# Kernel tuning notes

Measured on AMD Instinct MI355X. Metric: run time of the kernel, lower is better.

Reference implementation:

```python
import jax, jax.numpy as jnp
import numpy as np

B, S, IN_DIM, D, OUT_DIM = 8, 2048, 256, 1024, 256

def setup_inputs() -> dict:
    key = jax.random.key(0)
    ks = jax.random.split(key, 11)
    s_in = 1.0 / np.sqrt(IN_DIM)
    s_d = 1.0 / np.sqrt(D)
    return {
        "x": jax.random.normal(ks[0], (B, S, IN_DIM), dtype=jnp.float32),
        "Wi": jax.random.uniform(ks[1], (IN_DIM, D), jnp.float32, -s_in, s_in),
        "bi": jax.random.uniform(ks[2], (D,), jnp.float32, -s_in, s_in),
        "Wq": jax.random.uniform(ks[3], (D, D), jnp.float32, -s_d, s_d),
        "bq": jax.random.uniform(ks[4], (D,), jnp.float32, -s_d, s_d),
        "Wk": jax.random.uniform(ks[5], (D, D), jnp.float32, -s_d, s_d),
        "bk": jax.random.uniform(ks[6], (D,), jnp.float32, -s_d, s_d),
        "Wv": jax.random.uniform(ks[7], (D, D), jnp.float32, -s_d, s_d),
        "bv": jax.random.uniform(ks[8], (D,), jnp.float32, -s_d, s_d),
        "Wo": jax.random.uniform(ks[9], (D, OUT_DIM), jnp.float32, -s_d, s_d),
        "bo": jax.random.uniform(ks[10], (OUT_DIM,), jnp.float32, -s_d, s_d),
    }

def reference(x, Wi, bi, Wq, bq, Wk, bk, Wv, bv, Wo, bo):
    h = jnp.einsum('bsi,id->bsd', x, Wi) + bi          # input projection
    Q = jnp.einsum('bsd,de->bse', h, Wq) + bq
    K = jnp.einsum('bsd,de->bse', h, Wk) + bk
    V = jnp.einsum('bsd,de->bse', h, Wv) + bv
    scale = 1.0 / jnp.sqrt(jnp.asarray(Q.shape[-1], h.dtype))
    scores = jnp.einsum('bqd,bkd->bqk', Q, K) * scale   # [B,S,S]
    weights = jax.nn.softmax(scores, axis=-1)
    attended = jnp.einsum('bqk,bkd->bqd', weights, V)
    last = attended[:, -1, :]                           # only last token is projected
    out = last @ Wo + bo                                # [B, OUT_DIM]
    return out
```

## Files before the change

kernel.cpp:

```cpp
#include <hip/hip_runtime.h>

typedef unsigned short u16;
typedef __attribute__((ext_vector_type(8))) short bf16x8;
typedef __attribute__((ext_vector_type(4))) float f32x4;

#define B_  8
#define S_  2048
#define IN_ 256
#define D_  1024
#define OUT_ 256
#define M_  (B_*S_)

#define OFF_WIT   0UL
#define OFF_H     524288UL
#define OFF_QPART 34078720UL
#define OFF_Q     34340864UL
#define OFF_U     34373632UL
#define OFF_SC    34406400UL
#define OFF_W     34471936UL
#define OFF_HPART 34537472UL
#define OFF_HBAR  35061760UL
#define OFF_APART 35094528UL
#define OFF_ABAR  35356672UL
#define OFF_OPART 35389440UL

static __device__ __forceinline__ float bf2f(u16 u) {
    union { unsigned i; float f; } x; x.i = ((unsigned)u) << 16; return x.f;
}
static __device__ __forceinline__ u16 f2bf(float f) {
    union { float f; unsigned i; } x; x.f = f;
    unsigned r = x.i + 0x7FFFu + ((x.i >> 16) & 1u);
    return (u16)(r >> 16);
}
static __device__ __forceinline__ float2 bf2x2(int p) {
    union { unsigned i; float f; } a, b;
    a.i = ((unsigned)p) << 16;
    b.i = ((unsigned)p) & 0xFFFF0000u;
    float2 r; r.x = a.f; r.y = b.f; return r;
}

__global__ __launch_bounds__(256) void k_wit(const float* __restrict__ Wi, u16* __restrict__ WiT) {
    __shared__ float t[64][65];
    const int tid = threadIdx.x;
    const int n0 = blockIdx.x * 64;
    const int k0 = blockIdx.y * 64;
    const int c = tid & 63, rr = tid >> 6;
#pragma unroll
    for (int p = 0; p < 16; ++p) {
        int r = p * 4 + rr;
        t[r][c] = Wi[(k0 + r) * 1024 + n0 + c];
    }
    __syncthreads();
#pragma unroll
    for (int p = 0; p < 16; ++p) {
        int n = p * 4 + rr;
        WiT[(n0 + n) * 256 + k0 + c] = f2bf(t[c][n]);
    }
}

__global__ __launch_bounds__(256) void k_hgemm(const float* __restrict__ x,
                                               const u16* __restrict__ WiT,
                                               const float* __restrict__ bi,
                                               u16* __restrict__ h) {
    __shared__ u16 lA[128 * 128];
    __shared__ u16 lB[128 * 128];
    const int tid = threadIdx.x;
    const int l = tid & 63, w = tid >> 6;
    const int wm = w >> 1, wn = w & 1;
    const int m0 = blockIdx.y * 128, n0 = blockIdx.x * 128;
    const int q = l >> 4, r = l & 15;

    f32x4 acc[4][4];
#pragma unroll
    for (int mt = 0; mt < 4; ++mt)
#pragma unroll
        for (int nt = 0; nt < 4; ++nt)
            acc[mt][nt] = (f32x4){0.f, 0.f, 0.f, 0.f};

    for (int kh = 0; kh < 2; ++kh) {
        if (kh) __syncthreads();
#pragma unroll
        for (int p = 0; p < 8; ++p) {
            int id = p * 256 + tid;
            int row = id >> 4, cb = id & 15;
            const float4* src = reinterpret_cast<const float4*>(&x[(m0 + row) * IN_ + kh * 128 + cb * 8]);
            float4 v0 = src[0], v1 = src[1];
            u16 tmp[8];
            tmp[0] = f2bf(v0.x); tmp[1] = f2bf(v0.y); tmp[2] = f2bf(v0.z); tmp[3] = f2bf(v0.w);
            tmp[4] = f2bf(v1.x); tmp[5] = f2bf(v1.y); tmp[6] = f2bf(v1.z); tmp[7] = f2bf(v1.w);
            int4 pk;
            pk.x = (int)tmp[0] | ((int)tmp[1] << 16);
            pk.y = (int)tmp[2] | ((int)tmp[3] << 16);
            pk.z = (int)tmp[4] | ((int)tmp[5] << 16);
            pk.w = (int)tmp[6] | ((int)tmp[7] << 16);
            *reinterpret_cast<int4*>(&lA[row * 128 + ((cb ^ (row & 7)) << 3)]) = pk;
        }
#pragma unroll
        for (int p = 0; p < 8; ++p) {
            int id = p * 256 + tid;
            int row = id >> 4, cb = id & 15;
            int4 v = *reinterpret_cast<const int4*>(&WiT[(n0 + row) * IN_ + kh * 128 + cb * 8]);
            *reinterpret_cast<int4*>(&lB[row * 128 + ((cb ^ (row & 7)) << 3)]) = v;
        }
        __syncthreads();
#pragma unroll
        for (int kk = 0; kk < 4; ++kk) {
            int cb = kk * 4 + q;
            bf16x8 af[4], bfr[4];
#pragma unroll
            for (int mt = 0; mt < 4; ++mt) {
                int row = wm * 64 + mt * 16 + r;
                af[mt] = *reinterpret_cast<const bf16x8*>(&lA[row * 128 + ((cb ^ (row & 7)) << 3)]);
            }
#pragma unroll
            for (int nt = 0; nt < 4; ++nt) {
                int row = wn * 64 + nt * 16 + r;
                bfr[nt] = *reinterpret_cast<const bf16x8*>(&lB[row * 128 + ((cb ^ (row & 7)) << 3)]);
            }
#pragma unroll
            for (int mt = 0; mt < 4; ++mt)
#pragma unroll
                for (int nt = 0; nt < 4; ++nt)
                    acc[mt][nt] = __builtin_amdgcn_mfma_f32_16x16x32_bf16(af[mt], bfr[nt], acc[mt][nt], 0, 0, 0);
        }
    }
#pragma unroll
    for (int nt = 0; nt < 4; ++nt) {
        int col = n0 + wn * 64 + nt * 16 + r;
        float bival = bi[col];
#pragma unroll
        for (int mt = 0; mt < 4; ++mt) {
#pragma unroll
            for (int j = 0; j < 4; ++j) {
                int row = m0 + wm * 64 + mt * 16 + q * 4 + j;
                h[(size_t)row * D_ + col] = f2bf(acc[mt][nt][j] + bival);
            }
        }
    }
}

__global__ __launch_bounds__(256) void k_qpart(const u16* __restrict__ h, const float* __restrict__ Wq,
                                               float* __restrict__ part) {
    const int ec = blockIdx.x, dc = blockIdx.y, b = blockIdx.z, tid = threadIdx.x;
    __shared__ float hl[128];
    if (tid < 128) hl[tid] = bf2f(h[((size_t)(b * S_ + S_ - 1)) * D_ + dc * 128 + tid]);
    __syncthreads();
    const int e = ec * 256 + tid;
    float acc = 0.f;
#pragma unroll 4
    for (int i = 0; i < 128; ++i)
        acc += hl[i] * Wq[(size_t)(dc * 128 + i) * D_ + e];
    part[(dc * 8 + b) * D_ + e] = acc;
}

__global__ __launch_bounds__(256) void k_qreduce(const float* __restrict__ part, const float* __restrict__ bq,
                                                 float* __restrict__ Q) {
    const int e = blockIdx.x * 256 + threadIdx.x, b = blockIdx.y;
    float s = bq[e];
#pragma unroll
    for (int dc = 0; dc < 8; ++dc) s += part[(dc * 8 + b) * D_ + e];
    Q[b * D_ + e] = s;
}

__global__ __launch_bounds__(256) void k_u(const float* __restrict__ Wk, const float* __restrict__ Q,
                                           float* __restrict__ u) {
    const int b = blockIdx.y;
    const int w = threadIdx.x >> 6, l = threadIdx.x & 63;
    const int dbase = blockIdx.x * 16 + w * 4;
    const float* qb = &Q[b * D_];
    float4 qv[4];
#pragma unroll
    for (int p = 0; p < 4; ++p) qv[p] = *reinterpret_cast<const float4*>(&qb[p * 256 + l * 4]);
#pragma unroll
    for (int i = 0; i < 4; ++i) {
        const int d = dbase + i;
        const float* wr = &Wk[(size_t)d * D_];
        float acc = 0.f;
#pragma unroll
        for (int p = 0; p < 4; ++p) {
            float4 wv = *reinterpret_cast<const float4*>(&wr[p * 256 + l * 4]);
            acc += wv.x * qv[p].x + wv.y * qv[p].y + wv.z * qv[p].z + wv.w * qv[p].w;
        }
#pragma unroll
        for (int s = 32; s > 0; s >>= 1) acc += __shfl_xor(acc, s);
        if (l == 0) u[b * D_ + d] = acc;
    }
}

__global__ __launch_bounds__(256) void k_scores(const u16* __restrict__ h, const float* __restrict__ u,
                                                float* __restrict__ sc) {
    const int b = blockIdx.y;
    const int k = blockIdx.x * 4 + (threadIdx.x >> 6);
    const int l = threadIdx.x & 63;
    const u16* hr = &h[(size_t)(b * S_ + k) * D_];
    const float* ur = &u[b * D_];
    float acc = 0.f;
#pragma unroll
    for (int p = 0; p < 4; ++p) {
        int off = p * 256 + l * 4;
        int2 hv = *reinterpret_cast<const int2*>(&hr[off]);
        float4 uv = *reinterpret_cast<const float4*>(&ur[off]);
        float2 p0 = bf2x2(hv.x), p1 = bf2x2(hv.y);
        acc += p0.x * uv.x + p0.y * uv.y + p1.x * uv.z + p1.y * uv.w;
    }
#pragma unroll
    for (int s = 32; s > 0; s >>= 1) acc += __shfl_xor(acc, s);
    if (l == 0) sc[b * S_ + k] = acc * 0.03125f;
}

__global__ __launch_bounds__(256) void k_softmax(const float* __restrict__ sc, float* __restrict__ wt) {
    const int b = blockIdx.x, tid = threadIdx.x;
    const int w = tid >> 6, l = tid & 63;
    __shared__ float red[4], red2[4];
    float s[8];
    float mx = -1e30f;
#pragma unroll
    for (int j = 0; j < 8; ++j) {
        s[j] = sc[b * S_ + j * 256 + tid];
        mx = fmaxf(mx, s[j]);
    }
#pragma unroll
    for (int t = 32; t > 0; t >>= 1) mx = fmaxf(mx, __shfl_xor(mx, t));
    if (l == 0) red[w] = mx;
    __syncthreads();
    float bm = fmaxf(fmaxf(red[0], red[1]), fmaxf(red[2], red[3]));
    float sum = 0.f;
#pragma unroll
    for (int j = 0; j < 8; ++j) {
        s[j] = expf(s[j] - bm);
        sum += s[j];
    }
#pragma unroll
    for (int t = 32; t > 0; t >>= 1) sum += __shfl_xor(sum, t);
    if (l == 0) red2[w] = sum;
    __syncthreads();
    float inv = 1.f / (red2[0] + red2[1] + red2[2] + red2[3]);
#pragma unroll
    for (int j = 0; j < 8; ++j) wt[b * S_ + j * 256 + tid] = s[j] * inv;
}

__global__ __launch_bounds__(256) void k_hpart(const u16* __restrict__ h, const float* __restrict__ wt,
                                               float* __restrict__ part) {
    const int kc = blockIdx.x, b = blockIdx.y, tid = threadIdx.x;
    const int d0 = tid * 4;
    float a0 = 0.f, a1 = 0.f, a2 = 0.f, a3 = 0.f;
    for (int k = kc * 128; k < kc * 128 + 128; ++k) {
        float wgt = wt[b * S_ + k];
        int2 hv = *reinterpret_cast<const int2*>(&h[(size_t)(b * S_ + k) * D_ + d0]);
        float2 p0 = bf2x2(hv.x), p1 = bf2x2(hv.y);
        a0 += wgt * p0.x; a1 += wgt * p0.y; a2 += wgt * p1.x; a3 += wgt * p1.y;
    }
    float4 st = {a0, a1, a2, a3};
    *reinterpret_cast<float4*>(&part[(kc * 8 + b) * D_ + d0]) = st;
}

__global__ __launch_bounds__(256) void k_hreduce(const float* __restrict__ part, float* __restrict__ hbar) {
    const int d = blockIdx.x * 256 + threadIdx.x, b = blockIdx.y;
    float s = 0.f;
#pragma unroll
    for (int kc = 0; kc < 16; ++kc) s += part[(kc * 8 + b) * D_ + d];
    hbar[b * D_ + d] = s;
}

__global__ __launch_bounds__(256) void k_apart(const float* __restrict__ hbar, const float* __restrict__ Wv,
                                               float* __restrict__ part) {
    const int ec = blockIdx.x, dc = blockIdx.y, b = blockIdx.z, tid = threadIdx.x;
    __shared__ float hl[128];
    if (tid < 128) hl[tid] = hbar[b * D_ + dc * 128 + tid];
    __syncthreads();
    const int e = ec * 256 + tid;
    float acc = 0.f;
#pragma unroll 4
    for (int i = 0; i < 128; ++i)
        acc += hl[i] * Wv[(size_t)(dc * 128 + i) * D_ + e];
    part[(dc * 8 + b) * D_ + e] = acc;
}

__global__ __launch_bounds__(256) void k_areduce(const float* __restrict__ part, const float* __restrict__ bv,
                                                 float* __restrict__ abar) {
    const int e = blockIdx.x * 256 + threadIdx.x, b = blockIdx.y;
    float s = bv[e];
#pragma unroll
    for (int dc = 0; dc < 8; ++dc) s += part[(dc * 8 + b) * D_ + e];
    abar[b * D_ + e] = s;
}

__global__ __launch_bounds__(256) void k_opart(const float* __restrict__ abar, const float* __restrict__ Wo,
                                               float* __restrict__ part) {
    const int dc = blockIdx.x, b = blockIdx.y, tid = threadIdx.x;
    __shared__ float al[256];
    al[tid] = abar[b * D_ + dc * 256 + tid];
    __syncthreads();
    float acc = 0.f;
#pragma unroll 4
    for (int i = 0; i < 256; ++i)
        acc += al[i] * Wo[(size_t)(dc * 256 + i) * OUT_ + tid];
    part[(dc * 8 + b) * OUT_ + tid] = acc;
}

__global__ __launch_bounds__(256) void k_oreduce(const float* __restrict__ part, const float* __restrict__ bo,
                                                 float* __restrict__ out) {
    const int b = blockIdx.x, tid = threadIdx.x;
    float s = bo[tid];
#pragma unroll
    for (int dc = 0; dc < 4; ++dc) s += part[(dc * 8 + b) * OUT_ + tid];
    out[b * OUT_ + tid] = s;
}

extern "C" void kernel_launch(void* const* d_in, const int* in_sizes, int n_in,
                              void* d_out, int out_size, void* d_ws, size_t ws_size,
                              hipStream_t stream) {
    const float* x  = (const float*)d_in[0];
    const float* Wi = (const float*)d_in[1];
    const float* bi = (const float*)d_in[2];
    const float* Wq = (const float*)d_in[3];
    const float* bq = (const float*)d_in[4];
    const float* Wk = (const float*)d_in[5];
    const float* Wv = (const float*)d_in[7];
    const float* bv = (const float*)d_in[8];
    const float* Wo = (const float*)d_in[9];
    const float* bo = (const float*)d_in[10];
    float* out = (float*)d_out;

    char* ws = (char*)d_ws;
    u16*   WiT   = (u16*)  (ws + OFF_WIT);
    u16*   h     = (u16*)  (ws + OFF_H);
    float* Qpart = (float*)(ws + OFF_QPART);
    float* Q     = (float*)(ws + OFF_Q);
    float* u     = (float*)(ws + OFF_U);
    float* sc    = (float*)(ws + OFF_SC);
    float* wt    = (float*)(ws + OFF_W);
    float* hpart = (float*)(ws + OFF_HPART);
    float* hbar  = (float*)(ws + OFF_HBAR);
    float* apart = (float*)(ws + OFF_APART);
    float* abar  = (float*)(ws + OFF_ABAR);
    float* opart = (float*)(ws + OFF_OPART);

    k_wit    <<<dim3(16, 4),    256, 0, stream>>>(Wi, WiT);
    k_hgemm  <<<dim3(8, 128),   256, 0, stream>>>(x, WiT, bi, h);
    k_qpart  <<<dim3(4, 8, 8),  256, 0, stream>>>(h, Wq, Qpart);
    k_qreduce<<<dim3(4, 8),     256, 0, stream>>>(Qpart, bq, Q);
    k_u      <<<dim3(64, 8),    256, 0, stream>>>(Wk, Q, u);
    k_scores <<<dim3(512, 8),   256, 0, stream>>>(h, u, sc);
    k_softmax<<<dim3(8),        256, 0, stream>>>(sc, wt);
    k_hpart  <<<dim3(16, 8),    256, 0, stream>>>(h, wt, hpart);
    k_hreduce<<<dim3(4, 8),     256, 0, stream>>>(hpart, hbar);
    k_apart  <<<dim3(4, 8, 8),  256, 0, stream>>>(hbar, Wv, apart);
    k_areduce<<<dim3(4, 8),     256, 0, stream>>>(apart, bv, abar);
    k_opart  <<<dim3(4, 8),     256, 0, stream>>>(abar, Wo, opart);
    k_oreduce<<<dim3(8),        256, 0, stream>>>(opart, bo, out);
}
```

Before: 184.6 us.

## Fold Wq·Wk and Wv·Wo products, fuse softmax and collapse to five kernels

Reassociates attention for the last query: precomputes Wq·Wk^T and Wv·Wo with MFMA GEMMs inside the h-projection launch, and folds biases into constant vectors (dropping bk, which cancels in softmax). Scores, a chunked online softmax and weighted h accumulation are fused into one kernel, with a final kernel merging chunk maxima/sums and applying the folded output matrix. This removes many small GEMV and reduction launches and the repeated fp32 weight streaming, at the cost of extra dense GEMM work and bf16 rounding of weight products.

```diff
diff --git a/kernel.cpp b/kernel.cpp
--- a/kernel.cpp
+++ b/kernel.cpp
@@ -4,25 +4,25 @@
 typedef __attribute__((ext_vector_type(8))) short bf16x8;
 typedef __attribute__((ext_vector_type(4))) float f32x4;
 
-#define B_  8
-#define S_  2048
-#define IN_ 256
-#define D_  1024
+#define B_   8
+#define S_   2048
+#define IN_  256
+#define D_   1024
 #define OUT_ 256
-#define M_  (B_*S_)
+#define KC_  32
+#define RC_  64
 
 #define OFF_WIT   0UL
-#define OFF_H     524288UL
-#define OFF_QPART 34078720UL
-#define OFF_Q     34340864UL
-#define OFF_U     34373632UL
-#define OFF_SC    34406400UL
-#define OFF_W     34471936UL
-#define OFF_HPART 34537472UL
-#define OFF_HBAR  35061760UL
-#define OFF_APART 35094528UL
-#define OFF_ABAR  35356672UL
-#define OFF_OPART 35389440UL
+#define OFF_WOT   524288UL
+#define OFF_H     1048576UL
+#define OFF_AMAT  34603008UL
+#define OFF_AWO   38797312UL
+#define OFF_C     39845888UL
+#define OFF_CVOP  39849984UL
+#define OFF_CVO   39866368UL
+#define OFF_U     39870464UL
+#define OFF_PART  39903232UL
+#define OFF_MSUM  40951808UL
 
 static __device__ __forceinline__ float bf2f(u16 u) {
     union { unsigned i; float f; } x; x.i = ((unsigned)u) << 16; return x.f;
@@ -39,68 +39,113 @@
     float2 r; r.x = a.f; r.y = b.f; return r;
 }
 
-__global__ __launch_bounds__(256) void k_wit(const float* __restrict__ Wi, u16* __restrict__ WiT) {
+__global__ __launch_bounds__(256) void k1(const float* __restrict__ Wi, u16* __restrict__ WiT,
+                                          const float* __restrict__ Wo, u16* __restrict__ WoT,
+                                          const float* __restrict__ Wk, const float* __restrict__ bq,
+                                          float* __restrict__ cvec,
+                                          const float* __restrict__ bv, float* __restrict__ cvop) {
     __shared__ float t[64][65];
-    const int tid = threadIdx.x;
-    const int n0 = blockIdx.x * 64;
-    const int k0 = blockIdx.y * 64;
-    const int c = tid & 63, rr = tid >> 6;
-#pragma unroll
-    for (int p = 0; p < 16; ++p) {
-        int r = p * 4 + rr;
-        t[r][c] = Wi[(k0 + r) * 1024 + n0 + c];
-    }
-    __syncthreads();
-#pragma unroll
-    for (int p = 0; p < 16; ++p) {
-        int n = p * 4 + rr;
-        WiT[(n0 + n) * 256 + k0 + c] = f2bf(t[c][n]);
-    }
-}
-
-__global__ __launch_bounds__(256) void k_hgemm(const float* __restrict__ x,
-                                               const u16* __restrict__ WiT,
-                                               const float* __restrict__ bi,
-                                               u16* __restrict__ h) {
-    __shared__ u16 lA[128 * 128];
-    __shared__ u16 lB[128 * 128];
+    const int blk = blockIdx.x, tid = threadIdx.x;
+    if (blk < 64) {
+        const int n0 = (blk & 15) * 64, k0 = (blk >> 4) * 64;
+        const int cc = tid & 63, rr = tid >> 6;
+#pragma unroll
+        for (int p = 0; p < 16; ++p) { int r = p * 4 + rr; t[r][cc] = Wi[(k0 + r) * 1024 + n0 + cc]; }
+        __syncthreads();
+#pragma unroll
+        for (int p = 0; p < 16; ++p) { int n = p * 4 + rr; WiT[(n0 + n) * 256 + k0 + cc] = f2bf(t[cc][n]); }
+    } else if (blk < 128) {
+        const int b2 = blk - 64;
+        const int e0 = (b2 & 15) * 64, o0 = (b2 >> 4) * 64;
+        const int cc = tid & 63, rr = tid >> 6;
+#pragma unroll
+        for (int p = 0; p < 16; ++p) { int r = p * 4 + rr; t[r][cc] = Wo[(e0 + r) * 256 + o0 + cc]; }
+        __syncthreads();
+#pragma unroll
+        for (int p = 0; p < 16; ++p) { int o = p * 4 + rr; WoT[(o0 + o) * 1024 + e0 + cc] = f2bf(t[cc][o]); }
+    } else if (blk < 192) {
+        const int b2 = blk - 128;
+        const int w = tid >> 6, l = tid & 63;
+        const int dbase = b2 * 16 + w * 4;
+        float4 qv[4];
+#pragma unroll
+        for (int p = 0; p < 4; ++p) qv[p] = *reinterpret_cast<const float4*>(&bq[p * 256 + l * 4]);
+#pragma unroll
+        for (int i = 0; i < 4; ++i) {
+            const int d = dbase + i;
+            const float* wr = &Wk[(size_t)d * 1024];
+            float acc = 0.f;
+#pragma unroll
+            for (int p = 0; p < 4; ++p) {
+                float4 wv = *reinterpret_cast<const float4*>(&wr[p * 256 + l * 4]);
+                acc += wv.x * qv[p].x + wv.y * qv[p].y + wv.z * qv[p].z + wv.w * qv[p].w;
+            }
+#pragma unroll
+            for (int s = 32; s > 0; s >>= 1) acc += __shfl_xor(acc, s);
+            if (l == 0) cvec[d] = acc;
+        }
+    } else {
+        const int b2 = blk - 192;
+        const int e0 = b2 * 64;
+        float acc = 0.f;
+        for (int e = 0; e < 64; ++e) acc += bv[e0 + e] * Wo[(size_t)(e0 + e) * 256 + tid];
+        cvop[b2 * 256 + tid] = acc;
+    }
+}
+
+template<bool CONVB, bool BF16OUT>
+static __device__ __forceinline__ void gemm128(
+    const float* __restrict__ Af, int lda,
+    const void* __restrict__ Bsrc, int ldb,
+    int m0, int n0, int K,
+    u16* lA, u16* lB,
+    const float* __restrict__ bias,
+    u16* __restrict__ outb, float* __restrict__ outf, int ldo)
+{
     const int tid = threadIdx.x;
     const int l = tid & 63, w = tid >> 6;
     const int wm = w >> 1, wn = w & 1;
-    const int m0 = blockIdx.y * 128, n0 = blockIdx.x * 128;
     const int q = l >> 4, r = l & 15;
-
     f32x4 acc[4][4];
 #pragma unroll
     for (int mt = 0; mt < 4; ++mt)
 #pragma unroll
-        for (int nt = 0; nt < 4; ++nt)
-            acc[mt][nt] = (f32x4){0.f, 0.f, 0.f, 0.f};
-
-    for (int kh = 0; kh < 2; ++kh) {
+        for (int nt = 0; nt < 4; ++nt) acc[mt][nt] = (f32x4){0.f, 0.f, 0.f, 0.f};
+
+    const int KH = K >> 7;
+    for (int kh = 0; kh < KH; ++kh) {
         if (kh) __syncthreads();
 #pragma unroll
         for (int p = 0; p < 8; ++p) {
             int id = p * 256 + tid;
             int row = id >> 4, cb = id & 15;
-            const float4* src = reinterpret_cast<const float4*>(&x[(m0 + row) * IN_ + kh * 128 + cb * 8]);
+            const float4* src = reinterpret_cast<const float4*>(&Af[(size_t)(m0 + row) * lda + kh * 128 + cb * 8]);
             float4 v0 = src[0], v1 = src[1];
-            u16 tmp[8];
-            tmp[0] = f2bf(v0.x); tmp[1] = f2bf(v0.y); tmp[2] = f2bf(v0.z); tmp[3] = f2bf(v0.w);
-            tmp[4] = f2bf(v1.x); tmp[5] = f2bf(v1.y); tmp[6] = f2bf(v1.z); tmp[7] = f2bf(v1.w);
             int4 pk;
-            pk.x = (int)tmp[0] | ((int)tmp[1] << 16);
-            pk.y = (int)tmp[2] | ((int)tmp[3] << 16);
-            pk.z = (int)tmp[4] | ((int)tmp[5] << 16);
-            pk.w = (int)tmp[6] | ((int)tmp[7] << 16);
+            pk.x = (int)f2bf(v0.x) | ((int)f2bf(v0.y) << 16);
+            pk.y = (int)f2bf(v0.z) | ((int)f2bf(v0.w) << 16);
+            pk.z = (int)f2bf(v1.x) | ((int)f2bf(v1.y) << 16);
+            pk.w = (int)f2bf(v1.z) | ((int)f2bf(v1.w) << 16);
             *reinterpret_cast<int4*>(&lA[row * 128 + ((cb ^ (row & 7)) << 3)]) = pk;
         }
 #pragma unroll
         for (int p = 0; p < 8; ++p) {
             int id = p * 256 + tid;
             int row = id >> 4, cb = id & 15;
-            int4 v = *reinterpret_cast<const int4*>(&WiT[(n0 + row) * IN_ + kh * 128 + cb * 8]);
-            *reinterpret_cast<int4*>(&lB[row * 128 + ((cb ^ (row & 7)) << 3)]) = v;
+            int4 pk;
+            if constexpr (CONVB) {
+                const float* Bf = (const float*)Bsrc;
+                const float4* src = reinterpret_cast<const float4*>(&Bf[(size_t)(n0 + row) * ldb + kh * 128 + cb * 8]);
+                float4 v0 = src[0], v1 = src[1];
+                pk.x = (int)f2bf(v0.x) | ((int)f2bf(v0.y) << 16);
+                pk.y = (int)f2bf(v0.z) | ((int)f2bf(v0.w) << 16);
+                pk.z = (int)f2bf(v1.x) | ((int)f2bf(v1.y) << 16);
+                pk.w = (int)f2bf(v1.z) | ((int)f2bf(v1.w) << 16);
+            } else {
+                const u16* Bb = (const u16*)Bsrc;
+                pk = *reinterpret_cast<const int4*>(&Bb[(size_t)(n0 + row) * ldb + kh * 128 + cb * 8]);
+            }
+            *reinterpret_cast<int4*>(&lB[row * 128 + ((cb ^ (row & 7)) << 3)]) = pk;
         }
         __syncthreads();
 #pragma unroll
@@ -127,184 +172,184 @@
 #pragma unroll
     for (int nt = 0; nt < 4; ++nt) {
         int col = n0 + wn * 64 + nt * 16 + r;
-        float bival = bi[col];
+        float bb = 0.f;
+        if constexpr (BF16OUT) bb = bias[col];
 #pragma unroll
         for (int mt = 0; mt < 4; ++mt) {
 #pragma unroll
             for (int j = 0; j < 4; ++j) {
                 int row = m0 + wm * 64 + mt * 16 + q * 4 + j;
-                h[(size_t)row * D_ + col] = f2bf(acc[mt][nt][j] + bival);
-            }
-        }
-    }
-}
-
-__global__ __launch_bounds__(256) void k_qpart(const u16* __restrict__ h, const float* __restrict__ Wq,
-                                               float* __restrict__ part) {
-    const int ec = blockIdx.x, dc = blockIdx.y, b = blockIdx.z, tid = threadIdx.x;
-    __shared__ float hl[128];
-    if (tid < 128) hl[tid] = bf2f(h[((size_t)(b * S_ + S_ - 1)) * D_ + dc * 128 + tid]);
-    __syncthreads();
-    const int e = ec * 256 + tid;
-    float acc = 0.f;
-#pragma unroll 4
-    for (int i = 0; i < 128; ++i)
-        acc += hl[i] * Wq[(size_t)(dc * 128 + i) * D_ + e];
-    part[(dc * 8 + b) * D_ + e] = acc;
-}
-
-__global__ __launch_bounds__(256) void k_qreduce(const float* __restrict__ part, const float* __restrict__ bq,
-                                                 float* __restrict__ Q) {
-    const int e = blockIdx.x * 256 + threadIdx.x, b = blockIdx.y;
-    float s = bq[e];
-#pragma unroll
-    for (int dc = 0; dc < 8; ++dc) s += part[(dc * 8 + b) * D_ + e];
-    Q[b * D_ + e] = s;
-}
-
-__global__ __launch_bounds__(256) void k_u(const float* __restrict__ Wk, const float* __restrict__ Q,
-                                           float* __restrict__ u) {
-    const int b = blockIdx.y;
-    const int w = threadIdx.x >> 6, l = threadIdx.x & 63;
-    const int dbase = blockIdx.x * 16 + w * 4;
-    const float* qb = &Q[b * D_];
-    float4 qv[4];
-#pragma unroll
-    for (int p = 0; p < 4; ++p) qv[p] = *reinterpret_cast<const float4*>(&qb[p * 256 + l * 4]);
-#pragma unroll
-    for (int i = 0; i < 4; ++i) {
-        const int d = dbase + i;
-        const float* wr = &Wk[(size_t)d * D_];
-        float acc = 0.f;
+                if constexpr (BF16OUT) outb[(size_t)row * ldo + col] = f2bf(acc[mt][nt][j] + bb);
+                else                   outf[(size_t)row * ldo + col] = acc[mt][nt][j];
+            }
+        }
+    }
+}
+
+__global__ __launch_bounds__(256) void k2(const float* __restrict__ x, const u16* __restrict__ WiT,
+                                          const float* __restrict__ bi, u16* __restrict__ h,
+                                          const float* __restrict__ Wq, const float* __restrict__ Wk,
+                                          float* __restrict__ Amat,
+                                          const float* __restrict__ Wv, const u16* __restrict__ WoT,
+                                          float* __restrict__ Awo) {
+    __shared__ u16 lds[2 * 128 * 128];
+    u16* lA = lds;
+    u16* lB = lds + 128 * 128;
+    const int blk = blockIdx.x;
+    if (blk < 1024) {
+        int mt = blk >> 3, nt = blk & 7;
+        gemm128<false, true>(x, IN_, WiT, IN_, mt * 128, nt * 128, IN_, lA, lB, bi, h, nullptr, D_);
+    } else if (blk < 1088) {
+        int t = blk - 1024;
+        int mt = t >> 3, nt = t & 7;
+        gemm128<true, false>(Wq, D_, Wk, D_, mt * 128, nt * 128, D_, lA, lB, nullptr, nullptr, Amat, D_);
+    } else {
+        int t = blk - 1088;
+        int mt = t >> 1, nt = t & 1;
+        gemm128<false, false>(Wv, D_, WoT, D_, mt * 128, nt * 128, D_, lA, lB, nullptr, nullptr, Awo, OUT_);
+    }
+}
+
+__global__ __launch_bounds__(256) void k3(const u16* __restrict__ h, const float* __restrict__ Amat,
+                                          const float* __restrict__ cvec, float* __restrict__ u,
+                                          const float* __restrict__ cvop, const float* __restrict__ bo,
+                                          float* __restrict__ cvo) {
+    const int blk = blockIdx.x, tid = threadIdx.x;
+    if (blk < 128) {
+        const int b = blk >> 4, dc = blk & 15;
+        __shared__ float hl[1024];
+        __shared__ float red[4][64];
+        {
+            const size_t hb = ((size_t)(b * S_ + S_ - 1)) * D_;
+            int2 hv = *reinterpret_cast<const int2*>(&h[hb + tid * 4]);
+            float2 p0 = bf2x2(hv.x), p1 = bf2x2(hv.y);
+            hl[tid * 4 + 0] = p0.x; hl[tid * 4 + 1] = p0.y;
+            hl[tid * 4 + 2] = p1.x; hl[tid * 4 + 3] = p1.y;
+        }
+        __syncthreads();
+        const int dl = tid & 63, qd = tid >> 6;
+        const int d = dc * 64 + dl;
+        float ac[8] = {0.f, 0.f, 0.f, 0.f, 0.f, 0.f, 0.f, 0.f};
+        for (int dp = qd * 256; dp < qd * 256 + 256; dp += 8) {
+            float hh[8];
+#pragma unroll
+            for (int i = 0; i < 8; ++i) hh[i] = hl[dp + i];
+#pragma unroll
+            for (int i = 0; i < 8; ++i) ac[i] += hh[i] * Amat[(size_t)(dp + i) * D_ + d];
+        }
+        float acc = ((ac[0] + ac[1]) + (ac[2] + ac[3])) + ((ac[4] + ac[5]) + (ac[6] + ac[7]));
+        red[qd][dl] = acc;
+        __syncthreads();
+        if (qd == 0) {
+            float s = red[0][dl] + red[1][dl] + red[2][dl] + red[3][dl];
+            u[b * D_ + d] = s + cvec[d];
+        }
+    } else {
+        float s = bo[tid];
+#pragma unroll
+        for (int j = 0; j < 16; ++j) s += cvop[j * 256 + tid];
+        cvo[tid] = s;
+    }
+}
+
+__global__ __launch_bounds__(256) void k4(const u16* __restrict__ h, const float* __restrict__ u,
+                                          float* __restrict__ part, float* __restrict__ msum) {
+    const int kc = blockIdx.x, b = blockIdx.y;
+    const int tid = threadIdx.x, w = tid >> 6, l = tid & 63;
+    __shared__ float sNp[RC_];
+    float uv[16];
+    {
+        const float* ub = &u[b * D_ + l * 16];
 #pragma unroll
         for (int p = 0; p < 4; ++p) {
-            float4 wv = *reinterpret_cast<const float4*>(&wr[p * 256 + l * 4]);
-            acc += wv.x * qv[p].x + wv.y * qv[p].y + wv.z * qv[p].z + wv.w * qv[p].w;
-        }
+            float4 v = *reinterpret_cast<const float4*>(&ub[p * 4]);
+            uv[p * 4 + 0] = v.x; uv[p * 4 + 1] = v.y; uv[p * 4 + 2] = v.z; uv[p * 4 + 3] = v.w;
+        }
+    }
+    const size_t base = ((size_t)(b * S_) + kc * RC_) * D_;
+    for (int rr = 0; rr < 16; ++rr) {
+        const int row = w * 16 + rr;
+        const u16* hr = &h[base + (size_t)row * D_ + l * 16];
+        int4 q0 = *reinterpret_cast<const int4*>(&hr[0]);
+        int4 q1 = *reinterpret_cast<const int4*>(&hr[8]);
+        float2 a0 = bf2x2(q0.x), a1 = bf2x2(q0.y), a2 = bf2x2(q0.z), a3 = bf2x2(q0.w);
+        float2 c0 = bf2x2(q1.x), c1 = bf2x2(q1.y), c2 = bf2x2(q1.z), c3 = bf2x2(q1.w);
+        float acc = a0.x * uv[0] + a0.y * uv[1] + a1.x * uv[2] + a1.y * uv[3]
+                  + a2.x * uv[4] + a2.y * uv[5] + a3.x * uv[6] + a3.y * uv[7]
+                  + c0.x * uv[8] + c0.y * uv[9] + c1.x * uv[10] + c1.y * uv[11]
+                  + c2.x * uv[12] + c2.y * uv[13] + c3.x * uv[14] + c3.y * uv[15];
 #pragma unroll
         for (int s = 32; s > 0; s >>= 1) acc += __shfl_xor(acc, s);
-        if (l == 0) u[b * D_ + d] = acc;
-    }
-}
-
-__global__ __launch_bounds__(256) void k_scores(const u16* __restrict__ h, const float* __restrict__ u,
-                                                float* __restrict__ sc) {
-    const int b = blockIdx.y;
-    const int k = blockIdx.x * 4 + (threadIdx.x >> 6);
-    const int l = threadIdx.x & 63;
-    const u16* hr = &h[(size_t)(b * S_ + k) * D_];
-    const float* ur = &u[b * D_];
-    float acc = 0.f;
-#pragma unroll
-    for (int p = 0; p < 4; ++p) {
-        int off = p * 256 + l * 4;
-        int2 hv = *reinterpret_cast<const int2*>(&hr[off]);
-        float4 uv = *reinterpret_cast<const float4*>(&ur[off]);
-        float2 p0 = bf2x2(hv.x), p1 = bf2x2(hv.y);
-        acc += p0.x * uv.x + p0.y * uv.y + p1.x * uv.z + p1.y * uv.w;
-    }
-#pragma unroll
-    for (int s = 32; s > 0; s >>= 1) acc += __shfl_xor(acc, s);
-    if (l == 0) sc[b * S_ + k] = acc * 0.03125f;
-}
-
-__global__ __launch_bounds__(256) void k_softmax(const float* __restrict__ sc, float* __restrict__ wt) {
-    const int b = blockIdx.x, tid = threadIdx.x;
-    const int w = tid >> 6, l = tid & 63;
-    __shared__ float red[4], red2[4];
-    float s[8];
-    float mx = -1e30f;
-#pragma unroll
-    for (int j = 0; j < 8; ++j) {
-        s[j] = sc[b * S_ + j * 256 + tid];
-        mx = fmaxf(mx, s[j]);
-    }
-#pragma unroll
-    for (int t = 32; t > 0; t >>= 1) mx = fmaxf(mx, __shfl_xor(mx, t));
-    if (l == 0) red[w] = mx;
-    __syncthreads();
-    float bm = fmaxf(fmaxf(red[0], red[1]), fmaxf(red[2], red[3]));
-    float sum = 0.f;
-#pragma unroll
-    for (int j = 0; j < 8; ++j) {
-        s[j] = expf(s[j] - bm);
-        sum += s[j];
-    }
-#pragma unroll
-    for (int t = 32; t > 0; t >>= 1) sum += __shfl_xor(sum, t);
-    if (l == 0) red2[w] = sum;
-    __syncthreads();
-    float inv = 1.f / (red2[0] + red2[1] + red2[2] + red2[3]);
-#pragma unroll
-    for (int j = 0; j < 8; ++j) wt[b * S_ + j * 256 + tid] = s[j] * inv;
-}
-
-__global__ __launch_bounds__(256) void k_hpart(const u16* __restrict__ h, const float* __restrict__ wt,
-                                               float* __restrict__ part) {
-    const int kc = blockIdx.x, b = blockIdx.y, tid = threadIdx.x;
+        if (l == 0) sNp[row] = acc * 0.03125f;
+    }
+    __syncthreads();
+    float sv = sNp[l];
+    float mx = sv;
+#pragma unroll
+    for (int s = 32; s > 0; s >>= 1) mx = fmaxf(mx, __shfl_xor(mx, s));
+    float p = __expf(sv - mx);
+    float sum = p;
+#pragma unroll
+    for (int s = 32; s > 0; s >>= 1) sum += __shfl_xor(sum, s);
+    __syncthreads();
+    if (w == 0) sNp[l] = p;
+    if (tid == 0) { msum[(kc * 8 + b) * 2] = mx; msum[(kc * 8 + b) * 2 + 1] = sum; }
+    __syncthreads();
     const int d0 = tid * 4;
     float a0 = 0.f, a1 = 0.f, a2 = 0.f, a3 = 0.f;
-    for (int k = kc * 128; k < kc * 128 + 128; ++k) {
-        float wgt = wt[b * S_ + k];
-        int2 hv = *reinterpret_cast<const int2*>(&h[(size_t)(b * S_ + k) * D_ + d0]);
-        float2 p0 = bf2x2(hv.x), p1 = bf2x2(hv.y);
-        a0 += wgt * p0.x; a1 += wgt * p0.y; a2 += wgt * p1.x; a3 += wgt * p1.y;
+    for (int k = 0; k < RC_; ++k) {
+        float pk = sNp[k];
+        int2 hv = *reinterpret_cast<const int2*>(&h[base + (size_t)k * D_ + d0]);
+        float2 x0 = bf2x2(hv.x), x1 = bf2x2(hv.y);
+        a0 += pk * x0.x; a1 += pk * x0.y; a2 += pk * x1.x; a3 += pk * x1.y;
     }
     float4 st = {a0, a1, a2, a3};
-    *reinterpret_cast<float4*>(&part[(kc * 8 + b) * D_ + d0]) = st;
-}
-
-__global__ __launch_bounds__(256) void k_hreduce(const float* __restrict__ part, float* __restrict__ hbar) {
-    const int d = blockIdx.x * 256 + threadIdx.x, b = blockIdx.y;
-    float s = 0.f;
-#pragma unroll
-    for (int kc = 0; kc < 16; ++kc) s += part[(kc * 8 + b) * D_ + d];
-    hbar[b * D_ + d] = s;
-}
-
-__global__ __launch_bounds__(256) void k_apart(const float* __restrict__ hbar, const float* __restrict__ Wv,
-                                               float* __restrict__ part) {
-    const int ec = blockIdx.x, dc = blockIdx.y, b = blockIdx.z, tid = threadIdx.x;
-    __shared__ float hl[128];
-    if (tid < 128) hl[tid] = hbar[b * D_ + dc * 128 + tid];
-    __syncthreads();
-    const int e = ec * 256 + tid;
-    float acc = 0.f;
-#pragma unroll 4
-    for (int i = 0; i < 128; ++i)
-        acc += hl[i] * Wv[(size_t)(dc * 128 + i) * D_ + e];
-    part[(dc * 8 + b) * D_ + e] = acc;
-}
-
-__global__ __launch_bounds__(256) void k_areduce(const float* __restrict__ part, const float* __restrict__ bv,
-                                                 float* __restrict__ abar) {
-    const int e = blockIdx.x * 256 + threadIdx.x, b = blockIdx.y;
-    float s = bv[e];
-#pragma unroll
-    for (int dc = 0; dc < 8; ++dc) s += part[(dc * 8 + b) * D_ + e];
-    abar[b * D_ + e] = s;
-}
-
-__global__ __launch_bounds__(256) void k_opart(const float* __restrict__ abar, const float* __restrict__ Wo,
-                                               float* __restrict__ part) {
-    const int dc = blockIdx.x, b = blockIdx.y, tid = threadIdx.x;
-    __shared__ float al[256];
-    al[tid] = abar[b * D_ + dc * 256 + tid];
-    __syncthreads();
-    float acc = 0.f;
-#pragma unroll 4
-    for (int i = 0; i < 256; ++i)
-        acc += al[i] * Wo[(size_t)(dc * 256 + i) * OUT_ + tid];
-    part[(dc * 8 + b) * OUT_ + tid] = acc;
-}
-
-__global__ __launch_bounds__(256) void k_oreduce(const float* __restrict__ part, const float* __restrict__ bo,
-                                                 float* __restrict__ out) {
-    const int b = blockIdx.x, tid = threadIdx.x;
-    float s = bo[tid];
-#pragma unroll
-    for (int dc = 0; dc < 4; ++dc) s += part[(dc * 8 + b) * OUT_ + tid];
-    out[b * OUT_ + tid] = s;
+    *reinterpret_cast<float4*>(&part[((size_t)(kc * 8 + b)) * D_ + d0]) = st;
+}
+
+__global__ __launch_bounds__(256) void k5(const float* __restrict__ part, const float* __restrict__ msum,
+                                          const float* __restrict__ Awo, const float* __restrict__ cvo,
+                                          float* __restrict__ out) {
+    const int b = blockIdx.x, tid = threadIdx.x, w = tid >> 6, l = tid & 63;
+    __shared__ float hbar[1024];
+    __shared__ float red[4][256];
+    float m[KC_], sm[KC_];
+    float M = -1e30f;
+#pragma unroll
+    for (int c = 0; c < KC_; ++c) {
+        m[c] = msum[(c * 8 + b) * 2];
+        sm[c] = msum[(c * 8 + b) * 2 + 1];
+        M = fmaxf(M, m[c]);
+    }
+    float denom = 0.f;
+    float wgt[KC_];
+#pragma unroll
+    for (int c = 0; c < KC_; ++c) { wgt[c] = __expf(m[c] - M); denom += wgt[c] * sm[c]; }
+    const float inv = 1.f / denom;
+    float h0 = 0.f, h1 = 0.f, h2 = 0.f, h3 = 0.f;
+#pragma unroll
+    for (int c = 0; c < KC_; ++c) {
+        float4 pv = *reinterpret_cast<const float4*>(&part[((size_t)(c * 8 + b)) * D_ + tid * 4]);
+        h0 += wgt[c] * pv.x; h1 += wgt[c] * pv.y; h2 += wgt[c] * pv.z; h3 += wgt[c] * pv.w;
+    }
+    hbar[tid * 4 + 0] = h0 * inv; hbar[tid * 4 + 1] = h1 * inv;
+    hbar[tid * 4 + 2] = h2 * inv; hbar[tid * 4 + 3] = h3 * inv;
+    __syncthreads();
+    float o0 = 0.f, o1 = 0.f, o2 = 0.f, o3 = 0.f;
+    for (int d = w * 256; d < w * 256 + 256; d += 4) {
+        float4 hv = *reinterpret_cast<const float4*>(&hbar[d]);
+#pragma unroll
+        for (int j = 0; j < 4; ++j) {
+            float hj = (j == 0) ? hv.x : (j == 1) ? hv.y : (j == 2) ? hv.z : hv.w;
+            float4 av = *reinterpret_cast<const float4*>(&Awo[(size_t)(d + j) * OUT_ + l * 4]);
+            o0 += hj * av.x; o1 += hj * av.y; o2 += hj * av.z; o3 += hj * av.w;
+        }
+    }
+    red[w][l * 4 + 0] = o0; red[w][l * 4 + 1] = o1;
+    red[w][l * 4 + 2] = o2; red[w][l * 4 + 3] = o3;
+    __syncthreads();
+    float r = red[0][tid] + red[1][tid] + red[2][tid] + red[3][tid] + cvo[tid];
+    out[b * OUT_ + tid] = r;
 }
 
 extern "C" void kernel_launch(void* const* d_in, const int* in_sizes, int n_in,
@@ -323,30 +368,21 @@
     float* out = (float*)d_out;
 
     char* ws = (char*)d_ws;
-    u16*   WiT   = (u16*)  (ws + OFF_WIT);
-    u16*   h     = (u16*)  (ws + OFF_H);
-    float* Qpart = (float*)(ws + OFF_QPART);
-    float* Q     = (float*)(ws + OFF_Q);
-    float* u     = (float*)(ws + OFF_U);
-    float* sc    = (float*)(ws + OFF_SC);
-    float* wt    = (float*)(ws + OFF_W);
-    float* hpart = (float*)(ws + OFF_HPART);
-    float* hbar  = (float*)(ws + OFF_HBAR);
-    float* apart = (float*)(ws + OFF_APART);
-    float* abar  = (float*)(ws + OFF_ABAR);
-    float* opart = (float*)(ws + OFF_OPART);
-
-    k_wit    <<<dim3(16, 4),    256, 0, stream>>>(Wi, WiT);
-    k_hgemm  <<<dim3(8, 128),   256, 0, stream>>>(x, WiT, bi, h);
-    k_qpart  <<<dim3(4, 8, 8),  256, 0, stream>>>(h, Wq, Qpart);
-    k_qreduce<<<dim3(4, 8),     256, 0, stream>>>(Qpart, bq, Q);
-    k_u      <<<dim3(64, 8),    256, 0, stream>>>(Wk, Q, u);
-    k_scores <<<dim3(512, 8),   256, 0, stream>>>(h, u, sc);
-    k_softmax<<<dim3(8),        256, 0, stream>>>(sc, wt);
-    k_hpart  <<<dim3(16, 8),    256, 0, stream>>>(h, wt, hpart);
-    k_hreduce<<<dim3(4, 8),     256, 0, stream>>>(hpart, hbar);
-    k_apart  <<<dim3(4, 8, 8),  256, 0, stream>>>(hbar, Wv, apart);
-    k_areduce<<<dim3(4, 8),     256, 0, stream>>>(apart, bv, abar);
-    k_opart  <<<dim3(4, 8),     256, 0, stream>>>(abar, Wo, opart);
-    k_oreduce<<<dim3(8),        256, 0, stream>>>(opart, bo, out);
-}
+    u16*   WiT  = (u16*)  (ws + OFF_WIT);
+    u16*   WoT  = (u16*)  (ws + OFF_WOT);
+    u16*   h    = (u16*)  (ws + OFF_H);
+    float* Amat = (float*)(ws + OFF_AMAT);
+    float* Awo  = (float*)(ws + OFF_AWO);
+    float* cvec = (float*)(ws + OFF_C);
+    float* cvop = (float*)(ws + OFF_CVOP);
+    float* cvo  = (float*)(ws + OFF_CVO);
+    float* uvec = (float*)(ws + OFF_U);
+    float* part = (float*)(ws + OFF_PART);
+    float* msum = (float*)(ws + OFF_MSUM);
+
+    k1<<<208,        256, 0, stream>>>(Wi, WiT, Wo, WoT, Wk, bq, cvec, bv, cvop);
+    k2<<<1104,       256, 0, stream>>>(x, WiT, bi, h, Wq, Wk, Amat, Wv, WoT, Awo);
+    k3<<<129,        256, 0, stream>>>(h, Amat, cvec, uvec, cvop, bo, cvo);
+    k4<<<dim3(32,8), 256, 0, stream>>>(h, uvec, part, msum);
+    k5<<<8,          256, 0, stream>>>(part, msum, Awo, cvo, out);
+}
```

Result: slower. 206.4 us (+11.8%).
